# Performance work log

Measured on AMD Instinct MI355X. Metric: run time of the kernel, lower is better.

The kernel has to match this reference:

```python
import jax, jax.numpy as jnp
import numpy as np

GRAPH_BIAS_SCALE = 0.5
COMMITMENT_COST = 0.25

B, S, D, K = 32, 2048, 256, 2048  # batch, seq, latent_dim, n_symbols


def setup_inputs() -> dict:
    key = jax.random.key(0)
    k1, k2, k3, k4, k5 = jax.random.split(key, 5)
    return {
        "z_real": jax.random.normal(k1, (B, S, D), jnp.float32),
        "z_imag": jax.random.normal(k2, (B, S, D), jnp.float32),
        "prev_symbol_idx": jax.random.randint(k3, (B, S), 0, K),
        "codebook": jax.random.normal(k4, (K, 2 * D), jnp.float32),
        "adjacency": 0.1 * jax.random.normal(k5, (K, K), jnp.float32),
    }


def reference(z_real, z_imag, prev_symbol_idx, codebook, adjacency):
    # z_flat = cat([z.real, z.imag], -1) -> [B, S, 2D]
    z_flat = jnp.concatenate([z_real, z_imag], axis=-1)
    # squared-distance matrix to codebook: [B, S, K]
    d = (jnp.sum(z_flat ** 2, axis=-1, keepdims=True)
         + jnp.sum(codebook ** 2, axis=-1)
         - 2.0 * jnp.einsum("bsd,kd->bsk", z_flat, codebook))
    # graph prior bias from previous symbol
    graph_prior = adjacency[prev_symbol_idx]              # [B, S, K]
    d = d - GRAPH_BIAS_SCALE * jax.nn.sigmoid(graph_prior)
    min_indices = jnp.argmin(d, axis=-1)                  # [B, S]
    z_q = codebook[min_indices]                           # [B, S, 2D]
    loss_vq = jnp.mean((z_q - jax.lax.stop_gradient(z_flat)) ** 2)
    loss_commit = jnp.mean((jax.lax.stop_gradient(z_q) - z_flat) ** 2)
    loss = loss_vq + COMMITMENT_COST * loss_commit
    # straight-through estimator
    z_q_st = z_flat + jax.lax.stop_gradient(z_q - z_flat)
    half = z_q_st.shape[-1] // 2
    out_real = z_q_st[..., :half]
    out_imag = z_q_st[..., half:]
    return out_real, out_imag, loss, min_indices
```

## Files before the change

kernel.cpp:

```cpp
#include <hip/hip_runtime.h>
#include <math.h>

typedef _Float16 half8 __attribute__((ext_vector_type(8)));
typedef _Float16 half4v __attribute__((ext_vector_type(4)));
typedef float floatx4 __attribute__((ext_vector_type(4)));

constexpr int R_TOT = 65536;
constexpr int D     = 256;
constexpr int D2    = 512;
constexpr int K     = 2048;
constexpr float LOSS_SCALE = 1.25f / ((float)R_TOT * (float)D2);

__device__ __forceinline__ void async16(void* lds, const void* g) {
    __builtin_amdgcn_global_load_lds(
        (const __attribute__((address_space(1))) unsigned int*)g,
        (__attribute__((address_space(3))) unsigned int*)lds,
        16, 0, 0);
}

__global__ __launch_bounds__(256)
void k_split(const float* __restrict__ src, _Float16* __restrict__ dhi,
             _Float16* __restrict__ dlo, int coloff) {
    const int n4 = R_TOT * 64;
    for (int i = blockIdx.x * blockDim.x + threadIdx.x; i < n4;
         i += gridDim.x * blockDim.x) {
        int row = i >> 6, c4 = i & 63;
        float4 v = reinterpret_cast<const float4*>(src)[i];
        float vv[4] = {v.x, v.y, v.z, v.w};
        half4v h, l;
        #pragma unroll
        for (int j = 0; j < 4; ++j) {
            _Float16 hj = (_Float16)vv[j];
            h[j] = hj;
            l[j] = (_Float16)(vv[j] - (float)hj);
        }
        size_t di = (size_t)row * D2 + coloff + c4 * 4;
        *reinterpret_cast<half4v*>(dhi + di) = h;
        *reinterpret_cast<half4v*>(dlo + di) = l;
    }
}

__global__ __launch_bounds__(256)
void k_split_cb(const float* __restrict__ cb, _Float16* __restrict__ chi,
                _Float16* __restrict__ clo, float* __restrict__ cnorm) {
    int row  = blockIdx.x * 4 + (threadIdx.x >> 6);
    int lane = threadIdx.x & 63;
    const float4* p = reinterpret_cast<const float4*>(cb + (size_t)row * D2 + lane * 8);
    float s = 0.0f;
    #pragma unroll
    for (int q = 0; q < 2; ++q) {
        float4 v = p[q];
        float vv[4] = {v.x, v.y, v.z, v.w};
        half4v h, l;
        #pragma unroll
        for (int j = 0; j < 4; ++j) {
            _Float16 hj = (_Float16)vv[j];
            h[j] = hj;
            l[j] = (_Float16)(vv[j] - (float)hj);
            s += vv[j] * vv[j];
        }
        size_t di = (size_t)row * D2 + lane * 8 + q * 4;
        *reinterpret_cast<half4v*>(chi + di) = h;
        *reinterpret_cast<half4v*>(clo + di) = l;
    }
    #pragma unroll
    for (int o = 32; o > 0; o >>= 1) s += __shfl_down(s, o, 64);
    if (lane == 0) cnorm[row] = s;
}

__global__ __launch_bounds__(256)
void k_sigadj(const float* __restrict__ adj, float* __restrict__ sig) {
    const int n4 = K * K / 4;
    for (int i = blockIdx.x * blockDim.x + threadIdx.x; i < n4;
         i += gridDim.x * blockDim.x) {
        float4 v = reinterpret_cast<const float4*>(adj)[i];
        float4 o;
        o.x = 0.5f / (1.0f + __expf(-v.x));
        o.y = 0.5f / (1.0f + __expf(-v.y));
        o.z = 0.5f / (1.0f + __expf(-v.z));
        o.w = 0.5f / (1.0f + __expf(-v.w));
        reinterpret_cast<float4*>(sig)[i] = o;
    }
}

__global__ __launch_bounds__(256)
void k_score(const _Float16* __restrict__ z_hi, const _Float16* __restrict__ z_lo,
             const _Float16* __restrict__ c_hi, const _Float16* __restrict__ c_lo,
             const float* __restrict__ cnorm, const float* __restrict__ sigadj,
             const int* __restrict__ prev,
             float* __restrict__ ws_v, int* __restrict__ ws_i) {
    __shared__ _Float16 As[128 * 32] __attribute__((aligned(16)));
    __shared__ _Float16 Bs[128 * 32] __attribute__((aligned(16)));
    __shared__ float s_rv[128][2];
    __shared__ int   s_ri[128][2];

    const int tid  = threadIdx.x;
    const int w    = tid >> 6, lane = tid & 63;
    const int wr   = w >> 1,   wc   = w & 1;
    const int g    = lane >> 4, c   = lane & 15;
    const int row0 = blockIdx.x * 128;
    const int n0   = blockIdx.y * 512;

    int pidx[16];
    #pragma unroll
    for (int fm = 0; fm < 4; ++fm)
        #pragma unroll
        for (int j = 0; j < 4; ++j)
            pidx[fm * 4 + j] = prev[row0 + wr * 64 + fm * 16 + g * 4 + j];

    float bestv = 3.0e38f; int besti = 0;

    for (int nt = 0; nt < 4; ++nt) {
        floatx4 acc[4][4];
        #pragma unroll
        for (int i = 0; i < 4; ++i)
            #pragma unroll
            for (int j = 0; j < 4; ++j)
                acc[i][j] = (floatx4){0.f, 0.f, 0.f, 0.f};

        for (int ks = 0; ks < 48; ++ks) {
            const int seg = ks >> 4, kk = (ks & 15) * 32;
            const char* asrc = (const char*)((seg < 2 ? z_hi : z_lo)
                                             + (size_t)row0 * D2 + kk);
            const char* bsrc = (const char*)((seg == 1 ? c_lo : c_hi)
                                             + (size_t)(n0 + nt * 128) * D2 + kk);
            __syncthreads();
            #pragma unroll
            for (int r = 0; r < 2; ++r) {
                int slot = r * 4 + w;
                int o    = slot * 1024 + lane * 16;
                int trow = o >> 6, tcol = o & 63;
                size_t goff = (size_t)trow * 1024 + tcol;
                async16((char*)As + slot * 1024, asrc + goff);
                async16((char*)Bs + slot * 1024, bsrc + goff);
            }
            __syncthreads();

            half8 a[4], b[4];
            const half8* Av = (const half8*)As;
            const half8* Bv = (const half8*)Bs;
            #pragma unroll
            for (int f = 0; f < 4; ++f) {
                a[f] = Av[(wr * 64 + f * 16 + c) * 4 + g];
                b[f] = Bv[(wc * 64 + f * 16 + c) * 4 + g];
            }
            #pragma unroll
            for (int fm = 0; fm < 4; ++fm)
                #pragma unroll
                for (int fn = 0; fn < 4; ++fn)
                    acc[fm][fn] = __builtin_amdgcn_mfma_f32_16x16x32_f16(
                        a[fm], b[fn], acc[fm][fn], 0, 0, 0);
        }

        const int nbase = n0 + nt * 128 + wc * 64;
        float cn[4];
        #pragma unroll
        for (int fn = 0; fn < 4; ++fn) cn[fn] = cnorm[nbase + fn * 16 + c];
        #pragma unroll
        for (int fm = 0; fm < 4; ++fm) {
            #pragma unroll
            for (int j = 0; j < 4; ++j) {
                const float* srow = sigadj + (size_t)pidx[fm * 4 + j] * K;
                float bv = 3.0e38f; int bi = 0;
                #pragma unroll
                for (int fn = 0; fn < 4; ++fn) {
                    int col = nbase + fn * 16 + c;
                    float s = cn[fn] - 2.0f * acc[fm][fn][j] - srow[col];
                    if (s < bv || (s == bv && col < bi)) { bv = s; bi = col; }
                }
                #pragma unroll
                for (int m = 1; m < 16; m <<= 1) {
                    float ov = __shfl_xor(bv, m, 64);
                    int   oi = __shfl_xor(bi, m, 64);
                    if (ov < bv || (ov == bv && oi < bi)) { bv = ov; bi = oi; }
                }
                if (c == 0) {
                    int lr = wr * 64 + fm * 16 + g * 4 + j;
                    s_rv[lr][wc] = bv; s_ri[lr][wc] = bi;
                }
            }
        }
        __syncthreads();
        if (tid < 128) {
            float v0 = s_rv[tid][0], v1 = s_rv[tid][1];
            int   i0 = s_ri[tid][0], i1 = s_ri[tid][1];
            float nv; int ni;
            if (v0 < v1 || (v0 == v1 && i0 < i1)) { nv = v0; ni = i0; }
            else                                  { nv = v1; ni = i1; }
            if (nv < bestv || (nv == bestv && ni < besti)) { bestv = nv; besti = ni; }
        }
    }

    if (tid < 128) {
        int row = row0 + tid;
        ws_v[row * 4 + blockIdx.y] = bestv;
        ws_i[row * 4 + blockIdx.y] = besti;
    }
}

__global__ __launch_bounds__(256)
void k_final(const float* __restrict__ zr, const float* __restrict__ zi,
             const float* __restrict__ cb, const float* __restrict__ ws_v,
             const int* __restrict__ ws_i, float* __restrict__ out_real,
             float* __restrict__ out_imag, float* __restrict__ loss,
             float* __restrict__ out_idx) {
    __shared__ int s_kmin[128];
    const int tid  = threadIdx.x;
    const int row0 = blockIdx.x * 128;

    if (tid < 128) {
        int row = row0 + tid;
        float bv = ws_v[row * 4]; int bi = ws_i[row * 4];
        #pragma unroll
        for (int p = 1; p < 4; ++p) {
            float v = ws_v[row * 4 + p]; int idx = ws_i[row * 4 + p];
            if (v < bv || (v == bv && idx < bi)) { bv = v; bi = idx; }
        }
        s_kmin[tid] = bi;
        out_idx[row] = (float)bi;
    }
    __syncthreads();

    float lsum = 0.0f;
    for (int r = 0; r < 128; ++r) {
        int k  = s_kmin[r];
        int gr = row0 + r;
        float2 c2 = *(const float2*)(cb + (size_t)k * D2 + tid * 2);
        float2 z2; float* outp;
        if (tid < 128) {
            z2   = *(const float2*)(zr + (size_t)gr * D + tid * 2);
            outp = out_real + (size_t)gr * D + tid * 2;
        } else {
            z2   = *(const float2*)(zi + (size_t)gr * D + (tid - 128) * 2);
            outp = out_imag + (size_t)gr * D + (tid - 128) * 2;
        }
        *(float2*)outp = c2;
        float d0 = c2.x - z2.x, d1 = c2.y - z2.y;
        lsum += d0 * d0 + d1 * d1;
    }
    #pragma unroll
    for (int o = 32; o > 0; o >>= 1) lsum += __shfl_down(lsum, o, 64);
    __shared__ float s_ls[4];
    if ((tid & 63) == 0) s_ls[tid >> 6] = lsum;
    __syncthreads();
    if (tid == 0)
        atomicAdd(loss, (s_ls[0] + s_ls[1] + s_ls[2] + s_ls[3]) * LOSS_SCALE);
}

extern "C" void kernel_launch(void* const* d_in, const int* in_sizes, int n_in,
                              void* d_out, int out_size, void* d_ws, size_t ws_size,
                              hipStream_t stream) {
    const float* zr   = (const float*)d_in[0];
    const float* zi   = (const float*)d_in[1];
    const int*   prev = (const int*)  d_in[2];
    const float* cb   = (const float*)d_in[3];
    const float* adj  = (const float*)d_in[4];

    float* out      = (float*)d_out;
    float* out_real = out;
    float* out_imag = out + (size_t)R_TOT * D;
    float* loss     = out + (size_t)2 * R_TOT * D;
    float* out_idx  = loss + 1;

    char* w = (char*)d_ws;
    _Float16* z_hi  = (_Float16*)w;  w += (size_t)R_TOT * D2 * 2;
    _Float16* z_lo  = (_Float16*)w;  w += (size_t)R_TOT * D2 * 2;
    _Float16* c_hi  = (_Float16*)w;  w += (size_t)K * D2 * 2;
    _Float16* c_lo  = (_Float16*)w;  w += (size_t)K * D2 * 2;
    float*    cnorm = (float*)w;     w += (size_t)K * 4;
    float*    sigadj= (float*)w;     w += (size_t)K * K * 4;
    float*    ws_v  = (float*)w;     w += (size_t)R_TOT * 4 * 4;
    int*      ws_i  = (int*)w;       w += (size_t)R_TOT * 4 * 4;

    hipMemsetAsync(loss, 0, sizeof(float), stream);
    k_split   <<<2048, 256, 0, stream>>>(zr, z_hi, z_lo, 0);
    k_split   <<<2048, 256, 0, stream>>>(zi, z_hi, z_lo, 256);
    k_split_cb<<<K / 4, 256, 0, stream>>>(cb, c_hi, c_lo, cnorm);
    k_sigadj  <<<2048, 256, 0, stream>>>(adj, sigadj);
    k_score   <<<dim3(R_TOT / 128, 4), 256, 0, stream>>>(
        z_hi, z_lo, c_hi, c_lo, cnorm, sigadj, prev, ws_v, ws_i);
    k_final   <<<R_TOT / 128, 256, 0, stream>>>(
        zr, zi, cb, ws_v, ws_i, out_real, out_imag, loss, out_idx);
}
```

Before: 1.262 ms.

## Split score kernel into 128x128 tiles with 64-bit atomicMin argmin reduction

Each score block now computes a single 128-row by 128-code tile, and the grid grows from 512x4 to 16x512 blocks, so there is far more parallelism and each block runs one GEMM tile instead of four in sequence. Per-row argmin results merge across blocks through a 64-bit atomicMin on a packed key: the distance mapped to an order-preserving unsigned value in the high bits, the index in the low bits. This removes the shared-memory cross-wave merge and the four-way merge in the final kernel, at the cost of a memset of the key buffer and 16 atomics per row. The final kernel also switches to float4 loads and stores, handling two rows per iteration.

```diff
diff --git a/kernel.cpp b/kernel.cpp
--- a/kernel.cpp
+++ b/kernel.cpp
@@ -88,155 +88,129 @@
              const _Float16* __restrict__ c_hi, const _Float16* __restrict__ c_lo,
              const float* __restrict__ cnorm, const float* __restrict__ sigadj,
              const int* __restrict__ prev,
-             float* __restrict__ ws_v, int* __restrict__ ws_i) {
+             unsigned long long* __restrict__ ws_key) {
     __shared__ _Float16 As[128 * 32] __attribute__((aligned(16)));
     __shared__ _Float16 Bs[128 * 32] __attribute__((aligned(16)));
-    __shared__ float s_rv[128][2];
-    __shared__ int   s_ri[128][2];
 
     const int tid  = threadIdx.x;
     const int w    = tid >> 6, lane = tid & 63;
     const int wr   = w >> 1,   wc   = w & 1;
     const int g    = lane >> 4, c   = lane & 15;
-    const int row0 = blockIdx.x * 128;
-    const int n0   = blockIdx.y * 512;
-
-    int pidx[16];
-    #pragma unroll
-    for (int fm = 0; fm < 4; ++fm)
+    const int n0   = blockIdx.x * 128;
+    const int row0 = blockIdx.y * 128;
+
+    floatx4 acc[4][4];
+    #pragma unroll
+    for (int i = 0; i < 4; ++i)
         #pragma unroll
         for (int j = 0; j < 4; ++j)
-            pidx[fm * 4 + j] = prev[row0 + wr * 64 + fm * 16 + g * 4 + j];
-
-    float bestv = 3.0e38f; int besti = 0;
-
-    for (int nt = 0; nt < 4; ++nt) {
-        floatx4 acc[4][4];
-        #pragma unroll
-        for (int i = 0; i < 4; ++i)
+            acc[i][j] = (floatx4){0.f, 0.f, 0.f, 0.f};
+
+    for (int ks = 0; ks < 48; ++ks) {
+        const int seg = ks >> 4, kk = (ks & 15) * 32;
+        const char* asrc = (const char*)((seg < 2 ? z_hi : z_lo)
+                                         + (size_t)row0 * D2 + kk);
+        const char* bsrc = (const char*)((seg == 1 ? c_lo : c_hi)
+                                         + (size_t)n0 * D2 + kk);
+        __syncthreads();
+        #pragma unroll
+        for (int r = 0; r < 2; ++r) {
+            int slot = r * 4 + w;
+            int o    = slot * 1024 + lane * 16;
+            int trow = o >> 6, tcol = o & 63;
+            size_t goff = (size_t)trow * 1024 + tcol;
+            async16((char*)As + slot * 1024, asrc + goff);
+            async16((char*)Bs + slot * 1024, bsrc + goff);
+        }
+        __syncthreads();
+
+        half8 a[4], b[4];
+        const half8* Av = (const half8*)As;
+        const half8* Bv = (const half8*)Bs;
+        #pragma unroll
+        for (int f = 0; f < 4; ++f) {
+            a[f] = Av[(wr * 64 + f * 16 + c) * 4 + g];
+            b[f] = Bv[(wc * 64 + f * 16 + c) * 4 + g];
+        }
+        #pragma unroll
+        for (int fm = 0; fm < 4; ++fm)
             #pragma unroll
-            for (int j = 0; j < 4; ++j)
-                acc[i][j] = (floatx4){0.f, 0.f, 0.f, 0.f};
-
-        for (int ks = 0; ks < 48; ++ks) {
-            const int seg = ks >> 4, kk = (ks & 15) * 32;
-            const char* asrc = (const char*)((seg < 2 ? z_hi : z_lo)
-                                             + (size_t)row0 * D2 + kk);
-            const char* bsrc = (const char*)((seg == 1 ? c_lo : c_hi)
-                                             + (size_t)(n0 + nt * 128) * D2 + kk);
-            __syncthreads();
+            for (int fn = 0; fn < 4; ++fn)
+                acc[fm][fn] = __builtin_amdgcn_mfma_f32_16x16x32_f16(
+                    a[fm], b[fn], acc[fm][fn], 0, 0, 0);
+    }
+
+    const int nbase = n0 + wc * 64;
+    float cn[4];
+    #pragma unroll
+    for (int fn = 0; fn < 4; ++fn) cn[fn] = cnorm[nbase + fn * 16 + c];
+
+    #pragma unroll
+    for (int fm = 0; fm < 4; ++fm) {
+        #pragma unroll
+        for (int j = 0; j < 4; ++j) {
+            const int row = row0 + wr * 64 + fm * 16 + g * 4 + j;
+            const float* srow = sigadj + (size_t)prev[row] * K;
+            float bv = 3.0e38f; int bi = 0;
             #pragma unroll
-            for (int r = 0; r < 2; ++r) {
-                int slot = r * 4 + w;
-                int o    = slot * 1024 + lane * 16;
-                int trow = o >> 6, tcol = o & 63;
-                size_t goff = (size_t)trow * 1024 + tcol;
-                async16((char*)As + slot * 1024, asrc + goff);
-                async16((char*)Bs + slot * 1024, bsrc + goff);
-            }
-            __syncthreads();
-
-            half8 a[4], b[4];
-            const half8* Av = (const half8*)As;
-            const half8* Bv = (const half8*)Bs;
-            #pragma unroll
-            for (int f = 0; f < 4; ++f) {
-                a[f] = Av[(wr * 64 + f * 16 + c) * 4 + g];
-                b[f] = Bv[(wc * 64 + f * 16 + c) * 4 + g];
+            for (int fn = 0; fn < 4; ++fn) {
+                int col = nbase + fn * 16 + c;
+                float s = cn[fn] - 2.0f * acc[fm][fn][j] - srow[col];
+                if (s < bv || (s == bv && col < bi)) { bv = s; bi = col; }
             }
             #pragma unroll
-            for (int fm = 0; fm < 4; ++fm)
-                #pragma unroll
-                for (int fn = 0; fn < 4; ++fn)
-                    acc[fm][fn] = __builtin_amdgcn_mfma_f32_16x16x32_f16(
-                        a[fm], b[fn], acc[fm][fn], 0, 0, 0);
-        }
-
-        const int nbase = n0 + nt * 128 + wc * 64;
-        float cn[4];
-        #pragma unroll
-        for (int fn = 0; fn < 4; ++fn) cn[fn] = cnorm[nbase + fn * 16 + c];
-        #pragma unroll
-        for (int fm = 0; fm < 4; ++fm) {
-            #pragma unroll
-            for (int j = 0; j < 4; ++j) {
-                const float* srow = sigadj + (size_t)pidx[fm * 4 + j] * K;
-                float bv = 3.0e38f; int bi = 0;
-                #pragma unroll
-                for (int fn = 0; fn < 4; ++fn) {
-                    int col = nbase + fn * 16 + c;
-                    float s = cn[fn] - 2.0f * acc[fm][fn][j] - srow[col];
-                    if (s < bv || (s == bv && col < bi)) { bv = s; bi = col; }
-                }
-                #pragma unroll
-                for (int m = 1; m < 16; m <<= 1) {
-                    float ov = __shfl_xor(bv, m, 64);
-                    int   oi = __shfl_xor(bi, m, 64);
-                    if (ov < bv || (ov == bv && oi < bi)) { bv = ov; bi = oi; }
-                }
-                if (c == 0) {
-                    int lr = wr * 64 + fm * 16 + g * 4 + j;
-                    s_rv[lr][wc] = bv; s_ri[lr][wc] = bi;
-                }
+            for (int m = 1; m < 16; m <<= 1) {
+                float ov = __shfl_xor(bv, m, 64);
+                int   oi = __shfl_xor(bi, m, 64);
+                if (ov < bv || (ov == bv && oi < bi)) { bv = ov; bi = oi; }
             }
-        }
-        __syncthreads();
-        if (tid < 128) {
-            float v0 = s_rv[tid][0], v1 = s_rv[tid][1];
-            int   i0 = s_ri[tid][0], i1 = s_ri[tid][1];
-            float nv; int ni;
-            if (v0 < v1 || (v0 == v1 && i0 < i1)) { nv = v0; ni = i0; }
-            else                                  { nv = v1; ni = i1; }
-            if (nv < bestv || (nv == bestv && ni < besti)) { bestv = nv; besti = ni; }
-        }
-    }
-
-    if (tid < 128) {
-        int row = row0 + tid;
-        ws_v[row * 4 + blockIdx.y] = bestv;
-        ws_i[row * 4 + blockIdx.y] = besti;
+            if (c == 0) {
+                unsigned u = __float_as_uint(bv);
+                u = (u & 0x80000000u) ? ~u : (u | 0x80000000u);
+                unsigned long long key = ((unsigned long long)u << 32) | (unsigned)bi;
+                atomicMin(&ws_key[row], key);
+            }
+        }
     }
 }
 
 __global__ __launch_bounds__(256)
 void k_final(const float* __restrict__ zr, const float* __restrict__ zi,
-             const float* __restrict__ cb, const float* __restrict__ ws_v,
-             const int* __restrict__ ws_i, float* __restrict__ out_real,
-             float* __restrict__ out_imag, float* __restrict__ loss,
-             float* __restrict__ out_idx) {
+             const float* __restrict__ cb,
+             const unsigned long long* __restrict__ ws_key,
+             float* __restrict__ out_real, float* __restrict__ out_imag,
+             float* __restrict__ loss, float* __restrict__ out_idx) {
     __shared__ int s_kmin[128];
     const int tid  = threadIdx.x;
     const int row0 = blockIdx.x * 128;
 
     if (tid < 128) {
-        int row = row0 + tid;
-        float bv = ws_v[row * 4]; int bi = ws_i[row * 4];
-        #pragma unroll
-        for (int p = 1; p < 4; ++p) {
-            float v = ws_v[row * 4 + p]; int idx = ws_i[row * 4 + p];
-            if (v < bv || (v == bv && idx < bi)) { bv = v; bi = idx; }
-        }
+        unsigned long long key = ws_key[row0 + tid];
+        int bi = (int)(unsigned)(key & 0xFFFFFFFFu);
         s_kmin[tid] = bi;
-        out_idx[row] = (float)bi;
+        out_idx[row0 + tid] = (float)bi;
     }
     __syncthreads();
 
     float lsum = 0.0f;
-    for (int r = 0; r < 128; ++r) {
+    for (int it = 0; it < 64; ++it) {
+        int r  = it * 2 + (tid >> 7);
         int k  = s_kmin[r];
         int gr = row0 + r;
-        float2 c2 = *(const float2*)(cb + (size_t)k * D2 + tid * 2);
-        float2 z2; float* outp;
-        if (tid < 128) {
-            z2   = *(const float2*)(zr + (size_t)gr * D + tid * 2);
-            outp = out_real + (size_t)gr * D + tid * 2;
+        int q  = tid & 127;
+        float4 c4 = *(const float4*)(cb + (size_t)k * D2 + q * 4);
+        float4 z4; float* outp;
+        if (q < 64) {
+            z4   = *(const float4*)(zr + (size_t)gr * D + q * 4);
+            outp = out_real + (size_t)gr * D + q * 4;
         } else {
-            z2   = *(const float2*)(zi + (size_t)gr * D + (tid - 128) * 2);
-            outp = out_imag + (size_t)gr * D + (tid - 128) * 2;
-        }
-        *(float2*)outp = c2;
-        float d0 = c2.x - z2.x, d1 = c2.y - z2.y;
-        lsum += d0 * d0 + d1 * d1;
+            z4   = *(const float4*)(zi + (size_t)gr * D + (q - 64) * 4);
+            outp = out_imag + (size_t)gr * D + (q - 64) * 4;
+        }
+        *(float4*)outp = c4;
+        float dx = c4.x - z4.x, dy = c4.y - z4.y;
+        float dz = c4.z - z4.z, dw = c4.w - z4.w;
+        lsum += dx * dx + dy * dy + dz * dz + dw * dw;
     }
     #pragma unroll
     for (int o = 32; o > 0; o >>= 1) lsum += __shfl_down(lsum, o, 64);
@@ -269,16 +243,16 @@
     _Float16* c_lo  = (_Float16*)w;  w += (size_t)K * D2 * 2;
     float*    cnorm = (float*)w;     w += (size_t)K * 4;
     float*    sigadj= (float*)w;     w += (size_t)K * K * 4;
-    float*    ws_v  = (float*)w;     w += (size_t)R_TOT * 4 * 4;
-    int*      ws_i  = (int*)w;       w += (size_t)R_TOT * 4 * 4;
+    unsigned long long* ws_key = (unsigned long long*)w; w += (size_t)R_TOT * 8;
 
     hipMemsetAsync(loss, 0, sizeof(float), stream);
+    hipMemsetAsync(ws_key, 0xFF, (size_t)R_TOT * 8, stream);
     k_split   <<<2048, 256, 0, stream>>>(zr, z_hi, z_lo, 0);
     k_split   <<<2048, 256, 0, stream>>>(zi, z_hi, z_lo, 256);
     k_split_cb<<<K / 4, 256, 0, stream>>>(cb, c_hi, c_lo, cnorm);
     k_sigadj  <<<2048, 256, 0, stream>>>(adj, sigadj);
-    k_score   <<<dim3(R_TOT / 128, 4), 256, 0, stream>>>(
-        z_hi, z_lo, c_hi, c_lo, cnorm, sigadj, prev, ws_v, ws_i);
+    k_score   <<<dim3(16, 512), 256, 0, stream>>>(
+        z_hi, z_lo, c_hi, c_lo, cnorm, sigadj, prev, ws_key);
     k_final   <<<R_TOT / 128, 256, 0, stream>>>(
-        zr, zi, cb, ws_v, ws_i, out_real, out_imag, loss, out_idx);
-}
+        zr, zi, cb, ws_key, out_real, out_imag, loss, out_idx);
+}
```

After: 1.049 ms. 16.9% less time.
